# Optimization experiments

Hardware: AMD Instinct MI355X
Metric: run time of the kernel (lower is better)

## Reference

```python
import jax, jax.numpy as jnp
import numpy as np

B, T, D, H = 512, 300, 200, 128  # batch, seq_len, input_size, lstm hidden


def setup_inputs():
    key = jax.random.key(0)
    ks = jax.random.split(key, 24)
    inp = {}
    inp['b_x'] = jax.random.normal(ks[0], (B, T, D), jnp.float32)
    inp['b_y'] = jax.random.randint(ks[1], (B,), 0, 4)
    np.random.seed(1)  # matches torch module's fixed initial hidden state h_f
    inp['h_f'] = jnp.asarray(np.random.rand(H), jnp.float32)
    s = 0.05
    i = 2
    # PyTorch LSTM params per (layer, direction): W_ih [4H,din], W_hh [4H,H], b_ih, b_hh
    for tag, din in [('l0f', D), ('l0b', D), ('l1f', 2 * H), ('l1b', 2 * H)]:
        inp['w_ih_' + tag] = jax.random.normal(ks[i], (4 * H, din)) * s; i += 1
        inp['w_hh_' + tag] = jax.random.normal(ks[i], (4 * H, H)) * s; i += 1
        inp['b_ih_' + tag] = jax.random.normal(ks[i], (4 * H,)) * s; i += 1
        inp['b_hh_' + tag] = jax.random.normal(ks[i], (4 * H,)) * s; i += 1
    inp['w_l1'] = jax.random.normal(ks[18], (H, 2 * H + D)) * s  # [128,456], no bias
    inp['w_l2'] = jax.random.normal(ks[19], (4, H)) * s
    inp['b_l2'] = jax.random.normal(ks[20], (4,)) * s
    return inp


def _lstm_dir(x, w_ih, w_hh, b_ih, b_hh, h0, c0, reverse):
    # x: [T,B,din]; returns per-step hidden states [T,B,H] (PyTorch gate order i,f,g,o)
    if reverse:
        x = x[::-1]
    xp = jnp.einsum('tbd,gd->tbg', x, w_ih) + b_ih + b_hh  # precompute input projections

    def step(carry, xt):
        h, c = carry
        g = xt + h @ w_hh.T
        i, f, cc, o = jnp.split(g, 4, axis=-1)
        c = jax.nn.sigmoid(f) * c + jax.nn.sigmoid(i) * jnp.tanh(cc)
        h = jax.nn.sigmoid(o) * jnp.tanh(c)
        return (h, c), h

    _, hs = jax.lax.scan(step, (h0, c0), xp)
    return hs[::-1] if reverse else hs


def _forward(b_x, h_f, w_ih_l0f, w_hh_l0f, b_ih_l0f, b_hh_l0f, w_ih_l0b, w_hh_l0b, b_ih_l0b, b_hh_l0b, w_ih_l1f, w_hh_l1f, b_ih_l1f, b_hh_l1f, w_ih_l1b, w_hh_l1b, b_ih_l1b, b_hh_l1b, w_l1, w_l2, b_l2):
    Bn, Tn, _ = b_x.shape
    h0 = jnp.broadcast_to(h_f, (Bn, H)).astype(b_x.dtype)
    c0 = h0  # torch code sets C_0 = H_0
    xT = b_x.transpose(1, 0, 2)  # [T,B,D]
    # layer 0 (bidirectional)
    f0 = _lstm_dir(xT, w_ih_l0f, w_hh_l0f, b_ih_l0f, b_hh_l0f, h0, c0, False)
    r0 = _lstm_dir(xT, w_ih_l0b, w_hh_l0b, b_ih_l0b, b_hh_l0b, h0, c0, True)
    y0 = jnp.concatenate([f0, r0], axis=-1)  # [T,B,2H]
    # layer 1 (bidirectional)
    f1 = _lstm_dir(y0, w_ih_l1f, w_hh_l1f, b_ih_l1f, b_hh_l1f, h0, c0, False)
    r1 = _lstm_dir(y0, w_ih_l1b, w_hh_l1b, b_ih_l1b, b_hh_l1b, h0, c0, True)
    fw = f1.transpose(1, 0, 2)  # [B,T,H] forward-direction outputs
    bw = r1.transpose(1, 0, 2)  # [B,T,H] backward-direction outputs
    # rep_text (all lengths == T with randn inputs):
    # mat_FW[:,0] = h_f, mat_FW[:,l>=1] = fw[:,l]
    mat_FW = fw.at[:, 0, :].set(h_f.astype(fw.dtype))
    # mat_BW[:,k] = bw[:, T-2-k] for k<T-1 (time-reversed), mat_BW[:,T-1] = h_f
    mat_BW = jnp.concatenate([bw[:, Tn - 2::-1, :], jnp.broadcast_to(h_f, (Bn, 1, H)).astype(bw.dtype)], axis=1)
    data = jnp.concatenate([mat_FW, b_x, mat_BW], axis=-1)  # [B,T,456]
    h = jnp.tanh(jnp.einsum('btf,of->bto', data, w_l1))
    pooled = h.max(axis=1)  # MaxPool1d over full length
    return pooled @ w_l2.T + b_l2  # [B,4]


def reference(b_x, b_y, h_f, w_ih_l0f, w_hh_l0f, b_ih_l0f, b_hh_l0f, w_ih_l0b, w_hh_l0b, b_ih_l0b, b_hh_l0b, w_ih_l1f, w_hh_l1f, b_ih_l1f, b_hh_l1f, w_ih_l1b, w_hh_l1b, b_ih_l1b, b_hh_l1b, w_l1, w_l2, b_l2):
    outputs = _forward(b_x, h_f, w_ih_l0f, w_hh_l0f, b_ih_l0f, b_hh_l0f, w_ih_l0b, w_hh_l0b, b_ih_l0b, b_hh_l0b, w_ih_l1f, w_hh_l1f, b_ih_l1f, b_hh_l1f, w_ih_l1b, w_hh_l1b, b_ih_l1b, b_hh_l1b, w_l1, w_l2, b_l2)
    return outputs, b_y
```

## Files before the change

kernel.cpp:

```cpp
#include <hip/hip_runtime.h>

using u16 = unsigned short;
using u32 = unsigned int;
typedef __bf16 bf16x8 __attribute__((ext_vector_type(8)));
typedef float  f32x4  __attribute__((ext_vector_type(4)));
typedef u16    u16x8  __attribute__((ext_vector_type(8)));

__device__ __forceinline__ float b2f(u16 u) { return __uint_as_float(((u32)u) << 16); }
__device__ __forceinline__ u16 f2b(float f) {
    u32 u = __float_as_uint(f);
    u32 r = (u + 0x7fffu + ((u >> 16) & 1u)) >> 16;
    return (u16)r;
}
__device__ __forceinline__ float sigm(float x)      { return 1.f / (1.f + __expf(-x)); }
__device__ __forceinline__ float tanh_fast(float x) { return 1.f - 2.f / (__expf(2.f * x) + 1.f); }


#define NSEG 20
struct CvtArgs {
    const void* src[NSEG];
    u32 cnt[NSEG];
    u32 off[NSEG];
    u32 blk0[NSEG];
};

__global__ __launch_bounds__(256) void prep_k(
    CvtArgs a, const void* bx_src, const void* hf_src,
    u16* arena, u16* bxT, int* flag, int CV)
{
    const int tid = threadIdx.x;
    __shared__ int s_isb;
    if (tid == 0) s_isb = 1;
    __syncthreads();
    if (tid < 128) {
        float v = b2f(((const u16*)hf_src)[tid]);
        if (!(v >= 0.0f && v <= 1.0f)) atomicAnd(&s_isb, 0);
    }
    __syncthreads();
    const int isb = s_isb;
    const u32 blk = blockIdx.x;

    if (blk < (u32)CV) {
        int seg = 0;
#pragma unroll
        for (int i = 1; i < NSEG; ++i) if (blk >= a.blk0[i]) seg = i;
        const u32 base = (blk - a.blk0[seg]) * 2048u + tid * 8u;
        const u32 cnt = a.cnt[seg];
        u16* dst = arena + a.off[seg];
        if (isb) {
            const u16* s = (const u16*)a.src[seg];
            if (base + 8 <= cnt)      *(uint4*)(dst + base) = *(const uint4*)(s + base);
            else if (base < cnt)      for (u32 i = base; i < cnt; ++i) dst[i] = s[i];
        } else {
            const float* s = (const float*)a.src[seg];
            if (base + 8 <= cnt) {
                float4 f0 = *(const float4*)(s + base);
                float4 f1 = *(const float4*)(s + base + 4);
                u16x8 o;
                o[0]=f2b(f0.x); o[1]=f2b(f0.y); o[2]=f2b(f0.z); o[3]=f2b(f0.w);
                o[4]=f2b(f1.x); o[5]=f2b(f1.y); o[6]=f2b(f1.z); o[7]=f2b(f1.w);
                *(uint4*)(dst + base) = __builtin_bit_cast(uint4, o);
            } else if (base < cnt) {
                for (u32 i = base; i < cnt; ++i) dst[i] = f2b(s[i]);
            }
        }
    } else if (blk < (u32)CV + 15000u) {
        u32 i = (blk - CV) * 256 + tid;
        u32 dc = i % 25u, r = i / 25u;
        u32 t = r % 300u, b = r / 300u;
        size_t so = (size_t)r * 200 + dc * 8;
        size_t dofs = ((size_t)t * 512 + b) * 200 + dc * 8;
        u16x8 o;
        if (isb) {
            o = __builtin_bit_cast(u16x8, *(const uint4*)((const u16*)bx_src + so));
        } else {
            const float* s = (const float*)bx_src + so;
            float4 f0 = *(const float4*)s, f1 = *(const float4*)(s + 4);
            o[0]=f2b(f0.x); o[1]=f2b(f0.y); o[2]=f2b(f0.z); o[3]=f2b(f0.w);
            o[4]=f2b(f1.x); o[5]=f2b(f1.y); o[6]=f2b(f1.z); o[7]=f2b(f1.w);
        }
        *(uint4*)(bxT + dofs) = __builtin_bit_cast(uint4, o);
    } else {
        if (tid == 0) *flag = isb;
    }
}

template<int K>
__global__ __launch_bounds__(256) void proj_k(
    const u16* __restrict__ A0,
    const u16* __restrict__ W0, const u16* __restrict__ W1,
    const u16* __restrict__ bih0, const u16* __restrict__ bhh0,
    const u16* __restrict__ bih1, const u16* __restrict__ bhh1,
    u16* __restrict__ C0, u16* __restrict__ C1,
    int TL, int mb_f, int mb_b, int tb0_f, int tb0_b)
{
    constexpr int nK = (K + 31) / 32;
    __shared__ u16 As[128][40];
    __shared__ u16 Bs[128][40];

    const int tid = threadIdx.x;
    const int ntile = blockIdx.x & 7;
    const int dir = ntile >> 2, gnt = ntile & 3;
    const int mtile = (dir ? mb_b : mb_f) + (blockIdx.x >> 3);
    const int tb0 = dir ? tb0_b : tb0_f;
    const u16* W   = dir ? W1 : W0;
    const u16* bih = dir ? bih1 : bih0;
    const u16* bhh = dir ? bhh1 : bhh0;
    u16* C = dir ? C1 : C0;
    const int m0 = mtile * 128, n0 = gnt * 128;
    const int lane = tid & 63, wid = tid >> 6;
    const int wrow = wid >> 1, wcol = wid & 1;
    const int col = lane & 15, quad = lane >> 4;

    f32x4 acc[4][4] = {};

    for (int kt = 0; kt < nK; ++kt) {
        const int k0 = kt * 32;
#pragma unroll
        for (int it = 0; it < 2; ++it) {
            int idx = it * 256 + tid;
            int row = idx >> 2, ch = idx & 3;
            int k = k0 + ch * 8;
            uint4 av = {0,0,0,0}, bv = {0,0,0,0};
            if (k < K) {
                av = *(const uint4*)(A0 + (size_t)(m0 + row) * K + k);
                bv = *(const uint4*)(W  + (size_t)(n0 + row) * K + k);
            }
            *(uint4*)&As[row][ch * 8] = av;
            *(uint4*)&Bs[row][ch * 8] = bv;
        }
        __syncthreads();

        bf16x8 af[4], bf[4];
#pragma unroll
        for (int mt = 0; mt < 4; ++mt)
            af[mt] = __builtin_bit_cast(bf16x8, *(uint4*)&As[wrow * 64 + mt * 16 + col][quad * 8]);
#pragma unroll
        for (int nt = 0; nt < 4; ++nt)
            bf[nt] = __builtin_bit_cast(bf16x8, *(uint4*)&Bs[wcol * 64 + nt * 16 + col][quad * 8]);
#pragma unroll
        for (int mt = 0; mt < 4; ++mt)
#pragma unroll
            for (int nt = 0; nt < 4; ++nt)
                acc[mt][nt] = __builtin_amdgcn_mfma_f32_16x16x32_bf16(af[mt], bf[nt], acc[mt][nt], 0, 0, 0);
        __syncthreads();
    }

    const int tl = (mtile >> 2) - tb0;
#pragma unroll
    for (int mt = 0; mt < 4; ++mt) {
        const int bg = ((m0 + wrow * 64 + mt * 16) >> 4) & 31;
#pragma unroll
        for (int j = 0; j < 2; ++j) {
            const int w = wcol * 2 + j;
            const int nA = n0 + w * 32 + col;
            const float bA = b2f(bih[nA]) + b2f(bhh[nA]);
            const float bB = b2f(bih[nA + 16]) + b2f(bhh[nA + 16]);
            u16x8 o;
#pragma unroll
            for (int rg = 0; rg < 4; ++rg) {
                o[rg]     = f2b(acc[mt][2 * j][rg] + bA);
                o[4 + rg] = f2b(acc[mt][2 * j + 1][rg] + bB);
            }
            size_t idx16 = (((size_t)gnt * TL + tl) * 512 + bg * 16 + w * 4 + quad) * 16 + col;
            *(uint4*)(C + idx16 * 8) = __builtin_bit_cast(uint4, o);
        }
    }
}

__global__ __launch_bounds__(256, 1) void lstm_k(
    const u16* __restrict__ xp_f, const u16* __restrict__ xp_b,
    const u16* __restrict__ whh_f, const u16* __restrict__ whh_b,
    const u16* __restrict__ hf,
    u16* __restrict__ out_f, u16* __restrict__ out_b,
    u16* __restrict__ hstate, float* __restrict__ cstate,
    int ostride_f, int ostride_b, int ooff_f, int ooff_b,
    int S, int s0, int tb0_f, int tb0_b, int first, int TL)
{
    const int tid = threadIdx.x;
    const int lane = tid & 63, w = tid >> 6;
    const int col = lane & 15, quad = lane >> 4;
    const int dir = blockIdx.x >> 7;
    const int bq = blockIdx.x & 127, b0 = bq * 4;
    const int bg = bq >> 2, qb = bq & 3;

    const u16* xp  = dir ? xp_b  : xp_f;
    const u16* whh = dir ? whh_b : whh_f;
    u16* outp      = dir ? out_b : out_f;
    const int ostride = dir ? ostride_b : ostride_f;
    const int ooff    = dir ? ooff_b    : ooff_f;
    const int tb0     = dir ? tb0_b     : tb0_f;

    __shared__ u16 hist[8][4][136];
    __shared__ float gbuf[4][520];

    bf16x8 wf[8][4];
#pragma unroll
    for (int a = 0; a < 8; ++a) {
        int g = a >> 1, cb = a & 1;
        int n = g * 128 + w * 32 + cb * 16 + col;
#pragma unroll
        for (int ks = 0; ks < 4; ++ks)
            wf[a][ks] = __builtin_bit_cast(bf16x8,
                *(const uint4*)(whh + (size_t)n * 128 + ks * 32 + quad * 8));
    }

    const int cell = tid >> 1;
    const int bh = (tid & 1) * 2;

    float c2[2];
    if (first) {
        for (int i = tid; i < 512; i += 256)
            hist[0][i >> 7][i & 127] = hf[i & 127];
        float v = b2f(hf[cell]);
        c2[0] = v; c2[1] = v;
    } else {
        for (int i = tid; i < 512; i += 256)
            hist[0][i >> 7][i & 127] =
                hstate[(size_t)dir * 65536 + (b0 + (i >> 7)) * 128 + (i & 127)];
#pragma unroll
        for (int j = 0; j < 2; ++j)
            c2[j] = cstate[(size_t)dir * 65536 + (b0 + bh + j) * 128 + cell];
    }
    __syncthreads();

    const size_t inv = ((size_t)(bg * 16 + (cell >> 5) * 4 + qb)) * 128
                     + (size_t)(cell & 15) * 8 + ((cell >> 4) & 1) * 4 + bh;
    auto xload = [&](int sl, u32* q) {
        int t = dir ? (299 - (s0 + sl)) : (s0 + sl);
        int tl = t - tb0;
#pragma unroll
        for (int g = 0; g < 4; ++g)
            q[g] = *(const u32*)(xp + (size_t)(g * TL + tl) * 65536 + inv);
    };

    u32 xq[4];
    xload(0, xq);

#pragma unroll 1
    for (int sl = 0; sl < S; ++sl) {
        const int cur = sl & 7, nxt = (sl + 1) & 7;

        u32 xn[4];
        if (sl + 1 < S) xload(sl + 1, xn);

        bf16x8 hfr[4];
#pragma unroll
        for (int ks = 0; ks < 4; ++ks)
            hfr[ks] = __builtin_bit_cast(bf16x8, *(uint4*)&hist[cur][col & 3][ks * 32 + quad * 8]);

        f32x4 acc[8] = {};
#pragma unroll
        for (int ks = 0; ks < 4; ++ks)
#pragma unroll
            for (int a = 0; a < 8; ++a)
                acc[a] = __builtin_amdgcn_mfma_f32_16x16x32_bf16(wf[a][ks], hfr[ks], acc[a], 0, 0, 0);

        if (col < 4) {
#pragma unroll
            for (int a = 0; a < 8; ++a) {
                int g = a >> 1, cb = a & 1;
                int row = g * 128 + w * 32 + cb * 16 + quad * 4;
                *(f32x4*)&gbuf[col][row] = acc[a];
            }
        }
        __syncthreads();

        float h2[2];
#pragma unroll
        for (int j = 0; j < 2; ++j) {
            float gi = gbuf[bh + j][0 * 128 + cell];
            float gf = gbuf[bh + j][1 * 128 + cell];
            float gc = gbuf[bh + j][2 * 128 + cell];
            float go = gbuf[bh + j][3 * 128 + cell];
            u16 xi = (u16)(xq[0] >> (j * 16));
            u16 xf = (u16)(xq[1] >> (j * 16));
            u16 xc = (u16)(xq[2] >> (j * 16));
            u16 xo = (u16)(xq[3] >> (j * 16));
            float ig = sigm(gi + b2f(xi));
            float fg = sigm(gf + b2f(xf));
            float cg = tanh_fast(gc + b2f(xc));
            float og = sigm(go + b2f(xo));
            float cn = fg * c2[j] + ig * cg;
            c2[j] = cn;
            h2[j] = og * tanh_fast(cn);
        }
        hist[nxt][bh + 0][cell] = f2b(h2[0]);
        hist[nxt][bh + 1][cell] = f2b(h2[1]);

#pragma unroll
        for (int g = 0; g < 4; ++g) xq[g] = xn[g];
        __syncthreads();

        if ((sl & 7) == 7) {
            const int fb = sl >> 3;
            const int fs = tid >> 5, be = (tid >> 3) & 3, ch = tid & 7;
            const int j = (fs + 7) & 7;
            const int s = s0 + fb * 8 + j;
            const int t = dir ? (299 - s) : s;
            uint4 v0 = *(uint4*)&hist[fs][be][ch * 16];
            uint4 v1 = *(uint4*)&hist[fs][be][ch * 16 + 8];
            u16* dst = outp + ((size_t)t * 512 + b0 + be) * ostride + ooff + ch * 16;
            *(uint4*)dst = v0;
            *(uint4*)(dst + 8) = v1;
        }
    }

    const int rem = S & 7;
    if (rem) {
        const int base_s = s0 + (S & ~7);
        const int fs = tid >> 5, be = (tid >> 3) & 3, ch = tid & 7;
        const int j = (fs + 7) & 7;
        if (j < rem) {
            const int s = base_s + j;
            const int t = dir ? (299 - s) : s;
            uint4 v0 = *(uint4*)&hist[fs][be][ch * 16];
            uint4 v1 = *(uint4*)&hist[fs][be][ch * 16 + 8];
            u16* dst = outp + ((size_t)t * 512 + b0 + be) * ostride + ooff + ch * 16;
            *(uint4*)dst = v0;
            *(uint4*)(dst + 8) = v1;
        }
    }

    for (int i = tid; i < 512; i += 256)
        hstate[(size_t)dir * 65536 + (b0 + (i >> 7)) * 128 + (i & 127)] =
            hist[S & 7][i >> 7][i & 127];
#pragma unroll
    for (int j = 0; j < 2; ++j)
        cstate[(size_t)dir * 65536 + (b0 + bh + j) * 128 + cell] = c2[j];
}

__global__ __launch_bounds__(256) void headpool_k(
    const u16* __restrict__ bxT, const u16* __restrict__ W,
    const u16* __restrict__ F1, const u16* __restrict__ R1,
    const u16* __restrict__ HF, const u16* __restrict__ W2,
    const u16* __restrict__ B2, const int* __restrict__ BY,
    void* __restrict__ out, const int* __restrict__ flag)
{
    constexpr int K = 456, nK = 15;
    __shared__ u16 As[128][40];
    __shared__ u16 Bs[128][40];
    __shared__ float redL[8][128];
    __shared__ float pmax[128];

    const int b = blockIdx.x;
    const int tid = threadIdx.x;
    const int lane = tid & 63, wid = tid >> 6;
    const int wrow = wid >> 1, wcol = wid & 1;
    const int col = lane & 15, quad = lane >> 4;

    float lm[4] = { -1e30f, -1e30f, -1e30f, -1e30f };

    for (int mtile = 0; mtile < 3; ++mtile) {
        f32x4 acc[4][4] = {};
        for (int kt = 0; kt < nK; ++kt) {
            const int k0 = kt * 32;
#pragma unroll
            for (int it = 0; it < 2; ++it) {
                int idx = it * 256 + tid;
                int row = idx >> 2, ch = idx & 3;
                int k = k0 + ch * 8;
                int t = mtile * 128 + row;
                uint4 av = {0,0,0,0}, bv = {0,0,0,0};
                if (k < K) {
                    if (t < 300) {
                        const u16* p;
                        if (k < 128)      p = (t == 0)   ? (HF + k) : (F1 + ((size_t)t * 512 + b) * 128 + k);
                        else if (k < 328) p = bxT + ((size_t)t * 512 + b) * 200 + (k - 128);
                        else { int j = k - 328;
                               p = (t == 299) ? (HF + j) : (R1 + ((size_t)(298 - t) * 512 + b) * 128 + j); }
                        av = *(const uint4*)p;
                    }
                    bv = *(const uint4*)(W + (size_t)row * K + k);
                }
                *(uint4*)&As[row][ch * 8] = av;
                *(uint4*)&Bs[row][ch * 8] = bv;
            }
            __syncthreads();

            bf16x8 af[4], bf[4];
#pragma unroll
            for (int mt = 0; mt < 4; ++mt)
                af[mt] = __builtin_bit_cast(bf16x8, *(uint4*)&As[wrow * 64 + mt * 16 + col][quad * 8]);
#pragma unroll
            for (int nt = 0; nt < 4; ++nt)
                bf[nt] = __builtin_bit_cast(bf16x8, *(uint4*)&Bs[wcol * 64 + nt * 16 + col][quad * 8]);
#pragma unroll
            for (int mt = 0; mt < 4; ++mt)
#pragma unroll
                for (int nt = 0; nt < 4; ++nt)
                    acc[mt][nt] = __builtin_amdgcn_mfma_f32_16x16x32_bf16(af[mt], bf[nt], acc[mt][nt], 0, 0, 0);
            __syncthreads();
        }
#pragma unroll
        for (int nt = 0; nt < 4; ++nt)
#pragma unroll
            for (int mt = 0; mt < 4; ++mt)
#pragma unroll
                for (int rg = 0; rg < 4; ++rg) {
                    int t = mtile * 128 + wrow * 64 + mt * 16 + quad * 4 + rg;
                    if (t < 300) lm[nt] = fmaxf(lm[nt], tanh_fast(acc[mt][nt][rg]));
                }
    }

#pragma unroll
    for (int nt = 0; nt < 4; ++nt)
        redL[wrow * 4 + quad][wcol * 64 + nt * 16 + col] = lm[nt];
    __syncthreads();
    if (tid < 128) {
        float m = redL[0][tid];
#pragma unroll
        for (int r = 1; r < 8; ++r) m = fmaxf(m, redL[r][tid]);
        pmax[tid] = m;
    }
    __syncthreads();
    const bool isb = (*flag != 0);
    if (tid < 4) {
        float s = b2f(B2[tid]);
#pragma unroll 8
        for (int k = 0; k < 128; ++k) s += pmax[k] * b2f(W2[tid * 128 + k]);
        if (isb) ((u16*)out)[b * 4 + tid] = f2b(s);
        else     ((float*)out)[b * 4 + tid] = s;
    }
    if (tid == 4) {
        if (isb) ((u16*)out)[2048 + b] = f2b((float)BY[b]);
        else     ((float*)out)[2048 + b] = (float)BY[b];
    }
}

__global__ void diag_k(void* out, float code) {
    ((float*)out)[1] = code;
    ((u16*)out)[0] = f2b(code);
}

extern "C" void kernel_launch(void* const* d_in, const int* in_sizes, int n_in,
                              void* d_out, int out_size, void* d_ws, size_t ws_size,
                              hipStream_t stream)
{
    const int* b_y = (const int*)d_in[1];

    static const u32 CNT21[21] = {
        30720000, 128,
        102400, 65536, 512, 512,
        102400, 65536, 512, 512,
        131072, 65536, 512, 512,
        131072, 65536, 512, 512,
        58368, 512, 4 };
    static const int SRC_IDX[21] = { 0, 2, 3,4,5,6, 7,8,9,10, 11,12,13,14, 15,16,17,18, 19, 20, 21 };
    u32 off[21];
    u32 o = 0;
    for (int i = 0; i < 21; ++i) { off[i] = o; o += (CNT21[i] + 7u) & ~7u; }
    const size_t ARENA_BYTES = 63024640;
    const size_t PIPE_OFF    = ARENA_BYTES + 256;

    const size_t SZ_Y0 = 78643200;
    const size_t SZ_H  = 39321600;
    auto need = [&](int CSv) -> size_t {
        return PIPE_OFF + 2ull * (size_t)CSv * 524288ull + SZ_Y0 + 2 * SZ_H + 786432;
    };
    int CS = 0;
    if      (ws_size >= need(300)) CS = 300;
    else if (ws_size >= need(75))  CS = 75;
    else if (ws_size >= need(25))  CS = 25;
    else if (ws_size >= need(5))   CS = 5;
    if (CS == 0) {
        diag_k<<<1, 1, 0, stream>>>(d_out, (float)(1000 + (int)(ws_size >> 20)));
        return;
    }
    const int NC = 300 / CS;
    const size_t XPC = (size_t)CS * 524288ull;

    char* ws = (char*)d_ws;
    u16* arena = (u16*)ws;
    int* flag  = (int*)(ws + ARENA_BYTES);
    char* pb = ws + PIPE_OFF;
    u16* xpf = (u16*)(pb);
    u16* xpb = (u16*)(pb + XPC);
    u16* y0  = (u16*)(pb + 2 * XPC);
    u16* f1  = (u16*)(pb + 2 * XPC + SZ_Y0);
    u16* r1  = (u16*)(pb + 2 * XPC + SZ_Y0 + SZ_H);
    u16* hst = (u16*)(pb + 2 * XPC + SZ_Y0 + 2 * SZ_H);
    float* cst = (float*)(pb + 2 * XPC + SZ_Y0 + 2 * SZ_H + 262144);

    const u16 *bxT = arena + off[0], *hf_a = arena + off[1];
    const u16 *wih_l0f = arena + off[2],  *whh_l0f = arena + off[3],  *bih_l0f = arena + off[4],  *bhh_l0f = arena + off[5];
    const u16 *wih_l0b = arena + off[6],  *whh_l0b = arena + off[7],  *bih_l0b = arena + off[8],  *bhh_l0b = arena + off[9];
    const u16 *wih_l1f = arena + off[10], *whh_l1f = arena + off[11], *bih_l1f = arena + off[12], *bhh_l1f = arena + off[13];
    const u16 *wih_l1b = arena + off[14], *whh_l1b = arena + off[15], *bih_l1b = arena + off[16], *bhh_l1b = arena + off[17];
    const u16 *wl1_a = arena + off[18], *wl2_a = arena + off[19], *bl2_a = arena + off[20];

    CvtArgs ca;
    u32 bk = 0;
    for (int i = 0; i < NSEG; ++i) {
        ca.src[i] = d_in[SRC_IDX[i + 1]];
        ca.cnt[i] = CNT21[i + 1];
        ca.off[i] = off[i + 1];
        ca.blk0[i] = bk;
        bk += (CNT21[i + 1] + 2047u) / 2048u;
    }
    prep_k<<<bk + 15000 + 1, 256, 0, stream>>>(ca, d_in[0], d_in[2],
                                               arena, (u16*)(arena + off[0]), flag, (int)bk);

    for (int c = 0; c < NC; ++c) {
        int tf0 = c * CS, tb0 = 300 - (c + 1) * CS;
        proj_k<200><<<CS * 32, 256, 0, stream>>>(bxT, wih_l0f, wih_l0b,
            bih_l0f, bhh_l0f, bih_l0b, bhh_l0b, xpf, xpb, CS, tf0 * 4, tb0 * 4, tf0, tb0);
        lstm_k<<<256, 256, 0, stream>>>(xpf, xpb, whh_l0f, whh_l0b, hf_a, y0, y0, hst, cst,
                                        256, 256, 0, 128, CS, c * CS, tf0, tb0, c == 0, CS);
    }
    for (int c = 0; c < NC; ++c) {
        int tf0 = c * CS, tb0 = 300 - (c + 1) * CS;
        proj_k<256><<<CS * 32, 256, 0, stream>>>(y0, wih_l1f, wih_l1b,
            bih_l1f, bhh_l1f, bih_l1b, bhh_l1b, xpf, xpb, CS, tf0 * 4, tb0 * 4, tf0, tb0);
        lstm_k<<<256, 256, 0, stream>>>(xpf, xpb, whh_l1f, whh_l1b, hf_a, f1, r1, hst, cst,
                                        128, 128, 0, 0, CS, c * CS, tf0, tb0, c == 0, CS);
    }
    headpool_k<<<512, 256, 0, stream>>>(bxT, wl1_a, f1, r1, hf_a, wl2_a, bl2_a, b_y, d_out, flag);
}
```

Measured before the change: 1.380 ms.

## Overlap next-chunk input projection with LSTM recurrence via fused double-buffered kernel

Merges the input-projection GEMM and the LSTM recurrence into one kernel launch. The first 256 blocks run the recurrence for chunk c while the extra blocks compute the projection for chunk c+1 into a second buffer. The aim is to fill idle CUs during the latency-bound recurrence and to cut launch count. The trade-offs are a smaller chunk size (75 instead of 300 when the workspace is large), so there are more sequential launches, extra workspace for double buffering, and launch_bounds(256,2) on the LSTM path, which may limit registers for its persistent weight fragments.

Measured after the change: 1.169 ms. -15.3%, faster.

```diff
diff --git a/kernel.cpp b/kernel.cpp
--- a/kernel.cpp
+++ b/kernel.cpp
@@ -86,7 +86,8 @@
 }
 
 template<int K>
-__global__ __launch_bounds__(256) void proj_k(
+__device__ __forceinline__ void proj_body(
+    int pblk, void* smraw,
     const u16* __restrict__ A0,
     const u16* __restrict__ W0, const u16* __restrict__ W1,
     const u16* __restrict__ bih0, const u16* __restrict__ bhh0,
@@ -95,13 +96,15 @@
     int TL, int mb_f, int mb_b, int tb0_f, int tb0_b)
 {
     constexpr int nK = (K + 31) / 32;
-    __shared__ u16 As[128][40];
-    __shared__ u16 Bs[128][40];
+    struct PS { u16 As[128][40]; u16 Bs[128][40]; };
+    PS& sm = *(PS*)smraw;
+    auto& As = sm.As;
+    auto& Bs = sm.Bs;
 
     const int tid = threadIdx.x;
-    const int ntile = blockIdx.x & 7;
+    const int ntile = pblk & 7;
     const int dir = ntile >> 2, gnt = ntile & 3;
-    const int mtile = (dir ? mb_b : mb_f) + (blockIdx.x >> 3);
+    const int mtile = (dir ? mb_b : mb_f) + (pblk >> 3);
     const int tb0 = dir ? tb0_b : tb0_f;
     const u16* W   = dir ? W1 : W0;
     const u16* bih = dir ? bih1 : bih0;
@@ -168,7 +171,22 @@
     }
 }
 
-__global__ __launch_bounds__(256, 1) void lstm_k(
+template<int K>
+__global__ __launch_bounds__(256) void proj_k(
+    const u16* __restrict__ A0,
+    const u16* __restrict__ W0, const u16* __restrict__ W1,
+    const u16* __restrict__ bih0, const u16* __restrict__ bhh0,
+    const u16* __restrict__ bih1, const u16* __restrict__ bhh1,
+    u16* __restrict__ C0, u16* __restrict__ C1,
+    int TL, int mb_f, int mb_b, int tb0_f, int tb0_b)
+{
+    __shared__ alignas(16) char smraw[20480];
+    proj_body<K>(blockIdx.x, smraw, A0, W0, W1, bih0, bhh0, bih1, bhh1,
+                 C0, C1, TL, mb_f, mb_b, tb0_f, tb0_b);
+}
+
+__device__ __forceinline__ void lstm_body(
+    int lblk, void* smraw,
     const u16* __restrict__ xp_f, const u16* __restrict__ xp_b,
     const u16* __restrict__ whh_f, const u16* __restrict__ whh_b,
     const u16* __restrict__ hf,
@@ -180,8 +198,8 @@
     const int tid = threadIdx.x;
     const int lane = tid & 63, w = tid >> 6;
     const int col = lane & 15, quad = lane >> 4;
-    const int dir = blockIdx.x >> 7;
-    const int bq = blockIdx.x & 127, b0 = bq * 4;
+    const int dir = lblk >> 7;
+    const int bq = lblk & 127, b0 = bq * 4;
     const int bg = bq >> 2, qb = bq & 3;
 
     const u16* xp  = dir ? xp_b  : xp_f;
@@ -191,8 +209,10 @@
     const int ooff    = dir ? ooff_b    : ooff_f;
     const int tb0     = dir ? tb0_b     : tb0_f;
 
-    __shared__ u16 hist[8][4][136];
-    __shared__ float gbuf[4][520];
+    struct LS { u16 hist[8][4][136]; float gbuf[4][520]; };
+    LS& sm = *(LS*)smraw;
+    auto& hist = sm.hist;
+    auto& gbuf = sm.gbuf;
 
     bf16x8 wf[8][4];
 #pragma unroll
@@ -328,6 +348,33 @@
 #pragma unroll
     for (int j = 0; j < 2; ++j)
         cstate[(size_t)dir * 65536 + (b0 + bh + j) * 128 + cell] = c2[j];
+}
+
+template<int K>
+__global__ __launch_bounds__(256, 2) void fused_k(
+    const u16* __restrict__ xp_f, const u16* __restrict__ xp_b,
+    const u16* __restrict__ whh_f, const u16* __restrict__ whh_b,
+    const u16* __restrict__ hf,
+    u16* __restrict__ out_f, u16* __restrict__ out_b,
+    u16* __restrict__ hstate, float* __restrict__ cstate,
+    int ostride_f, int ostride_b, int ooff_f, int ooff_b,
+    int S, int s0, int ltb0_f, int ltb0_b, int first, int TL,
+    const u16* __restrict__ A0,
+    const u16* __restrict__ W0, const u16* __restrict__ W1,
+    const u16* __restrict__ bih0, const u16* __restrict__ bhh0,
+    const u16* __restrict__ bih1, const u16* __restrict__ bhh1,
+    u16* __restrict__ C0, u16* __restrict__ C1,
+    int pmb_f, int pmb_b, int ptb0_f, int ptb0_b)
+{
+    __shared__ alignas(16) char smraw[20480];
+    if (blockIdx.x < 256) {
+        lstm_body(blockIdx.x, smraw, xp_f, xp_b, whh_f, whh_b, hf, out_f, out_b,
+                  hstate, cstate, ostride_f, ostride_b, ooff_f, ooff_b,
+                  S, s0, ltb0_f, ltb0_b, first, TL);
+    } else {
+        proj_body<K>(blockIdx.x - 256, smraw, A0, W0, W1, bih0, bhh0, bih1, bhh1,
+                     C0, C1, TL, pmb_f, pmb_b, ptb0_f, ptb0_b);
+    }
 }
 
 __global__ __launch_bounds__(256) void headpool_k(
@@ -455,32 +502,44 @@
 
     const size_t SZ_Y0 = 78643200;
     const size_t SZ_H  = 39321600;
-    auto need = [&](int CSv) -> size_t {
+    auto needD = [&](int CSv) -> size_t {
+        return PIPE_OFF + 4ull * (size_t)CSv * 524288ull + SZ_Y0 + 2 * SZ_H + 786432;
+    };
+    auto needS = [&](int CSv) -> size_t {
         return PIPE_OFF + 2ull * (size_t)CSv * 524288ull + SZ_Y0 + 2 * SZ_H + 786432;
     };
-    int CS = 0;
-    if      (ws_size >= need(300)) CS = 300;
-    else if (ws_size >= need(75))  CS = 75;
-    else if (ws_size >= need(25))  CS = 25;
-    else if (ws_size >= need(5))   CS = 5;
+    int CS = 0, dbuf = 1;
+    if      (ws_size >= needD(75)) CS = 75;
+    else if (ws_size >= needD(50)) CS = 50;
+    else if (ws_size >= needD(25)) CS = 25;
+    else if (ws_size >= needD(5))  CS = 5;
+    else {
+        dbuf = 0;
+        if      (ws_size >= needS(25)) CS = 25;
+        else if (ws_size >= needS(5))  CS = 5;
+    }
     if (CS == 0) {
         diag_k<<<1, 1, 0, stream>>>(d_out, (float)(1000 + (int)(ws_size >> 20)));
         return;
     }
     const int NC = 300 / CS;
     const size_t XPC = (size_t)CS * 524288ull;
+    const size_t XPTOT = (dbuf ? 4 : 2) * XPC;
 
     char* ws = (char*)d_ws;
     u16* arena = (u16*)ws;
     int* flag  = (int*)(ws + ARENA_BYTES);
     char* pb = ws + PIPE_OFF;
-    u16* xpf = (u16*)(pb);
-    u16* xpb = (u16*)(pb + XPC);
-    u16* y0  = (u16*)(pb + 2 * XPC);
-    u16* f1  = (u16*)(pb + 2 * XPC + SZ_Y0);
-    u16* r1  = (u16*)(pb + 2 * XPC + SZ_Y0 + SZ_H);
-    u16* hst = (u16*)(pb + 2 * XPC + SZ_Y0 + 2 * SZ_H);
-    float* cst = (float*)(pb + 2 * XPC + SZ_Y0 + 2 * SZ_H + 262144);
+    u16* xc_f[2]; u16* xc_b[2];
+    xc_f[0] = (u16*)(pb);
+    xc_b[0] = (u16*)(pb + XPC);
+    if (dbuf) { xc_f[1] = (u16*)(pb + 2 * XPC); xc_b[1] = (u16*)(pb + 3 * XPC); }
+    else      { xc_f[1] = xc_f[0];              xc_b[1] = xc_b[0]; }
+    u16* y0  = (u16*)(pb + XPTOT);
+    u16* f1  = (u16*)(pb + XPTOT + SZ_Y0);
+    u16* r1  = (u16*)(pb + XPTOT + SZ_Y0 + SZ_H);
+    u16* hst = (u16*)(pb + XPTOT + SZ_Y0 + 2 * SZ_H);
+    float* cst = (float*)(pb + XPTOT + SZ_Y0 + 2 * SZ_H + 262144);
 
     const u16 *bxT = arena + off[0], *hf_a = arena + off[1];
     const u16 *wih_l0f = arena + off[2],  *whh_l0f = arena + off[3],  *bih_l0f = arena + off[4],  *bhh_l0f = arena + off[5];
@@ -501,19 +560,43 @@
     prep_k<<<bk + 15000 + 1, 256, 0, stream>>>(ca, d_in[0], d_in[2],
                                                arena, (u16*)(arena + off[0]), flag, (int)bk);
 
+    proj_k<200><<<CS * 32, 256, 0, stream>>>(bxT, wih_l0f, wih_l0b,
+        bih_l0f, bhh_l0f, bih_l0b, bhh_l0b, xc_f[0], xc_b[0], CS, 0, (300 - CS) * 4, 0, 300 - CS);
     for (int c = 0; c < NC; ++c) {
-        int tf0 = c * CS, tb0 = 300 - (c + 1) * CS;
-        proj_k<200><<<CS * 32, 256, 0, stream>>>(bxT, wih_l0f, wih_l0b,
-            bih_l0f, bhh_l0f, bih_l0b, bhh_l0b, xpf, xpb, CS, tf0 * 4, tb0 * 4, tf0, tb0);
-        lstm_k<<<256, 256, 0, stream>>>(xpf, xpb, whh_l0f, whh_l0b, hf_a, y0, y0, hst, cst,
-                                        256, 256, 0, 128, CS, c * CS, tf0, tb0, c == 0, CS);
-    }
+        const int par = dbuf ? (c & 1) : 0;
+        const int nx  = dbuf ? (par ^ 1) : 0;
+        const int tf0 = c * CS, tb0 = 300 - (c + 1) * CS;
+        if (!dbuf && c > 0)
+            proj_k<200><<<CS * 32, 256, 0, stream>>>(bxT, wih_l0f, wih_l0b,
+                bih_l0f, bhh_l0f, bih_l0b, bhh_l0b, xc_f[0], xc_b[0], CS,
+                tf0 * 4, tb0 * 4, tf0, tb0);
+        const int dp = dbuf && (c + 1 < NC);
+        const int ntf0 = (c + 1) * CS, ntb0 = 300 - (c + 2) * CS;
+        fused_k<200><<<256 + (dp ? CS * 32 : 0), 256, 0, stream>>>(
+            xc_f[par], xc_b[par], whh_l0f, whh_l0b, hf_a, y0, y0, hst, cst,
+            256, 256, 0, 128, CS, c * CS, tf0, tb0, c == 0, CS,
+            bxT, wih_l0f, wih_l0b, bih_l0f, bhh_l0f, bih_l0b, bhh_l0b,
+            xc_f[nx], xc_b[nx], ntf0 * 4, ntb0 * 4, ntf0, ntb0);
+    }
+
+    proj_k<256><<<CS * 32, 256, 0, stream>>>(y0, wih_l1f, wih_l1b,
+        bih_l1f, bhh_l1f, bih_l1b, bhh_l1b, xc_f[0], xc_b[0], CS, 0, (300 - CS) * 4, 0, 300 - CS);
     for (int c = 0; c < NC; ++c) {
-        int tf0 = c * CS, tb0 = 300 - (c + 1) * CS;
-        proj_k<256><<<CS * 32, 256, 0, stream>>>(y0, wih_l1f, wih_l1b,
-            bih_l1f, bhh_l1f, bih_l1b, bhh_l1b, xpf, xpb, CS, tf0 * 4, tb0 * 4, tf0, tb0);
-        lstm_k<<<256, 256, 0, stream>>>(xpf, xpb, whh_l1f, whh_l1b, hf_a, f1, r1, hst, cst,
-                                        128, 128, 0, 0, CS, c * CS, tf0, tb0, c == 0, CS);
-    }
+        const int par = dbuf ? (c & 1) : 0;
+        const int nx  = dbuf ? (par ^ 1) : 0;
+        const int tf0 = c * CS, tb0 = 300 - (c + 1) * CS;
+        if (!dbuf && c > 0)
+            proj_k<256><<<CS * 32, 256, 0, stream>>>(y0, wih_l1f, wih_l1b,
+                bih_l1f, bhh_l1f, bih_l1b, bhh_l1b, xc_f[0], xc_b[0], CS,
+                tf0 * 4, tb0 * 4, tf0, tb0);
+        const int dp = dbuf && (c + 1 < NC);
+        const int ntf0 = (c + 1) * CS, ntb0 = 300 - (c + 2) * CS;
+        fused_k<256><<<256 + (dp ? CS * 32 : 0), 256, 0, stream>>>(
+            xc_f[par], xc_b[par], whh_l1f, whh_l1b, hf_a, f1, r1, hst, cst,
+            128, 128, 0, 0, CS, c * CS, tf0, tb0, c == 0, CS,
+            y0, wih_l1f, wih_l1b, bih_l1f, bhh_l1f, bih_l1b, bhh_l1b,
+            xc_f[nx], xc_b[nx], ntf0 * 4, ntb0 * 4, ntf0, ntb0);
+    }
+
     headpool_k<<<512, 256, 0, stream>>>(bxT, wl1_a, f1, r1, hf_a, wl2_a, bl2_a, b_y, d_out, flag);
 }
```
